# Optimization experiments

Measured on AMD Instinct MI355X. Metric: run time of the kernel, lower is better.

Reference implementation:

```python
import jax, jax.numpy as jnp
import numpy as np

B, T, V, E, H, NT = 64, 512, 8000, 256, 512, 4
HD = H // 2  # hidden per direction


def setup_inputs() -> dict:
    key = jax.random.key(0)
    ks = jax.random.split(key, 14)
    s = 0.1
    length = jnp.sort(jax.random.randint(ks[0], (B,), T // 2, T + 1))[::-1]  # sorted desc (pack_padded)
    mask = (jnp.arange(T)[None, :] < length[:, None]).astype(jnp.int32)
    sentence = jax.random.randint(ks[1], (B, T), 1, V + 1) * mask  # pad positions -> padding_idx 0
    tags = jax.random.randint(ks[2], (B, T), 0, NT)
    embedding = (jax.random.normal(ks[3], (V + 1, E)) * s).at[0].set(0.0)  # padding_idx row = 0
    w_ih_f = jax.random.normal(ks[4], (4 * HD, E)) * s
    w_hh_f = jax.random.normal(ks[5], (4 * HD, HD)) * s
    b_f = jax.random.normal(ks[6], (4 * HD,)) * s  # b_ih + b_hh combined
    w_ih_b = jax.random.normal(ks[7], (4 * HD, E)) * s
    w_hh_b = jax.random.normal(ks[8], (4 * HD, HD)) * s
    b_b = jax.random.normal(ks[9], (4 * HD,)) * s
    w_out = jax.random.normal(ks[10], (NT, H)) * s
    b_out = jnp.zeros((NT,), jnp.float32)
    start_trans = jax.random.uniform(ks[11], (NT,), minval=-0.1, maxval=0.1)
    end_trans = jax.random.uniform(ks[12], (NT,), minval=-0.1, maxval=0.1)
    trans = jax.random.uniform(ks[13], (NT, NT), minval=-0.1, maxval=0.1)
    return {"sentence": sentence, "tags": tags, "mask": mask, "length": length,
            "embedding": embedding, "w_ih_f": w_ih_f, "w_hh_f": w_hh_f, "b_f": b_f,
            "w_ih_b": w_ih_b, "w_hh_b": w_hh_b, "b_b": b_b,
            "w_out": w_out, "b_out": b_out,
            "start_trans": start_trans, "end_trans": end_trans, "trans": trans}


def _lstm_dir(x, maskf, w_ih, w_hh, b, reverse):
    # x: [B,T,E]; masked LSTM == packed LSTM (zero init state, padded outputs = 0)
    xg = jnp.einsum('bte,ge->btg', x, w_ih) + b           # [B,T,4HD]
    xg = jnp.swapaxes(xg, 0, 1)                           # [T,B,4HD]
    mt = jnp.swapaxes(maskf, 0, 1)[..., None]             # [T,B,1]
    h0 = jnp.zeros((x.shape[0], w_hh.shape[1]), x.dtype)

    def step(carry, inp):
        h, c = carry
        g, m = inp
        gates = g + h @ w_hh.T
        i, f, gg, o = jnp.split(gates, 4, axis=-1)  # torch gate order: i, f, g, o
        i = jax.nn.sigmoid(i); f = jax.nn.sigmoid(f)
        gg = jnp.tanh(gg); o = jax.nn.sigmoid(o)
        cn = f * c + i * gg
        hn = o * jnp.tanh(cn)
        h = m * hn + (1.0 - m) * h
        c = m * cn + (1.0 - m) * c
        return (h, c), h * m

    _, hs = jax.lax.scan(step, (h0, h0), (xg, mt), reverse=reverse)
    return jnp.swapaxes(hs, 0, 1)  # [B,T,HD]


def reference(sentence, tags, mask, length, embedding, w_ih_f, w_hh_f, b_f,
              w_ih_b, w_hh_b, b_b, w_out, b_out, start_trans, end_trans, trans):
    maskf = mask.astype(embedding.dtype)
    embeds = embedding[sentence]                           # [B,T,E] (dropout: eval/identity)
    hf = _lstm_dir(embeds, maskf, w_ih_f, w_hh_f, b_f, False)
    hb = _lstm_dir(embeds, maskf, w_ih_b, w_hh_b, b_b, True)
    feats = jnp.concatenate([hf, hb], -1) @ w_out.T + b_out  # [B,T,NT]

    # --- CRF log-likelihood (torchcrf), reduction='mean'; loss = -mean llh ---
    bsz = tags.shape[0]
    emit = jnp.take_along_axis(feats, tags[..., None], -1)[..., 0]   # [B,T]
    trans_sc = trans[tags[:, :-1], tags[:, 1:]]                       # [B,T-1]
    num = start_trans[tags[:, 0]] + emit[:, 0] \
        + jnp.sum(maskf[:, 1:] * (emit[:, 1:] + trans_sc), axis=1)
    last_tag = tags[jnp.arange(bsz), length - 1]
    num = num + end_trans[last_tag]

    ft = jnp.swapaxes(feats, 0, 1)                  # [T,B,NT]
    mt = jnp.swapaxes(maskf, 0, 1)[..., None]       # [T,B,1]
    alpha0 = start_trans[None, :] + ft[0]

    def step(alpha, inp):
        e, m = inp
        new = jax.nn.logsumexp(alpha[:, :, None] + trans[None] + e[:, None, :], axis=1)
        return m * new + (1.0 - m) * alpha, None

    alpha, _ = jax.lax.scan(step, alpha0, (ft[1:], mt[1:]))
    logZ = jax.nn.logsumexp(alpha + end_trans[None, :], axis=1)
    return -jnp.mean(num - logZ)
```

## Files before the change

kernel.cpp:

```cpp
#include <hip/hip_runtime.h>
#include <stdint.h>

#define BB 64
#define TT 512
#define EE 256
#define GG 1024
#define HDIM 256
#define NTAG 4

typedef _Float16 f16;
typedef _Float16 half8 __attribute__((ext_vector_type(8)));
typedef float floatx4 __attribute__((ext_vector_type(4)));

__device__ __forceinline__ int dot4i8(int a, int b, int c) {
#if __has_builtin(__builtin_amdgcn_sdot4)
  return __builtin_amdgcn_sdot4(a, b, c, false);
#else
  c += (int)(signed char)(a & 0xff)         * (int)(signed char)(b & 0xff);
  c += (int)(signed char)((a >> 8) & 0xff)  * (int)(signed char)((b >> 8) & 0xff);
  c += (int)(signed char)((a >> 16) & 0xff) * (int)(signed char)((b >> 16) & 0xff);
  c += (int)(signed char)((a >> 24) & 0xff) * (int)(signed char)((b >> 24) & 0xff);
  return c;
#endif
}

__device__ __forceinline__ float sigm(float x) {
  x = fminf(fmaxf(x, -30.f), 30.f);
  return 1.f / (1.f + __expf(-x));
}
__device__ __forceinline__ float tanh_f(float x) {
  x = fminf(fmaxf(x, -15.f), 15.f);
  float e = __expf(-2.f * x);
  return (1.f - e) / (1.f + e);
}

__global__ void pack_kernel(const float* __restrict__ wihf, const float* __restrict__ wihb,
                            const float* __restrict__ whhf, const float* __restrict__ whhb,
                            f16* __restrict__ bmat, uint32_t* __restrict__ whhp,
                            float* __restrict__ swhh) {
  int wv = (blockIdx.x * 256 + threadIdx.x) >> 6;
  int lane = threadIdx.x & 63;
  if (wv >= 2048) return;
  int dir = wv >> 10;
  int g = wv & 1023;
  const float* wih = dir ? wihb : wihf;
  const float* src = wih + (size_t)g * EE + lane * 4;
  f16* bp = bmat + (size_t)wv * EE + lane * 4;
  floatx4 v = *(const floatx4*)src;
  bp[0] = (f16)v[0]; bp[1] = (f16)v[1]; bp[2] = (f16)v[2]; bp[3] = (f16)v[3];
  const float* whh = dir ? whhb : whhf;
  floatx4 w = *(const floatx4*)(whh + (size_t)g * EE + lane * 4);
  float am = fmaxf(fmaxf(fabsf(w[0]), fabsf(w[1])), fmaxf(fabsf(w[2]), fabsf(w[3])));
#pragma unroll
  for (int d = 1; d < 64; d <<= 1) am = fmaxf(am, __shfl_xor(am, d));
  float s = am * (1.f / 127.f);
  float inv = am > 0.f ? 127.f / am : 0.f;
  int q0 = (int)rintf(w[0] * inv);
  int q1 = (int)rintf(w[1] * inv);
  int q2 = (int)rintf(w[2] * inv);
  int q3 = (int)rintf(w[3] * inv);
  uint32_t p = (uint32_t)(q0 & 255) | ((uint32_t)(q1 & 255) << 8) |
               ((uint32_t)(q2 & 255) << 16) | ((uint32_t)(q3 & 255) << 24);
  whhp[dir * 65536 + lane * 1024 + g] = p;
  if (lane == 0) swhh[dir * 1024 + g] = s;
}

__global__ __launch_bounds__(256) void gemm_kernel(
    const int* __restrict__ sentence, const float* __restrict__ embedding,
    const f16* __restrict__ bmat, f16* __restrict__ xgF, f16* __restrict__ xgB,
    int t0f, int t0b, int L, int Lsh) {
  __shared__ __attribute__((aligned(16))) f16 As[128][72];
  __shared__ __attribute__((aligned(16))) f16 Bs[128][72];
  int rt = blockIdx.x;
  int nt = blockIdx.y;
  int tid = threadIdx.x;
  int lane = tid & 63;
  int wv = tid >> 6;
  int BL = BB * L;
  int rbase = rt * 128;
  int half = (rbase >= BL) ? 1 : 0;
  int rloc0 = rbase - half * BL;
  int t0 = half ? t0b : t0f;

  floatx4 acc[4][4];
#pragma unroll
  for (int i = 0; i < 4; ++i)
#pragma unroll
    for (int j = 0; j < 4; ++j) acc[i][j] = (floatx4){0.f, 0.f, 0.f, 0.f};

  int ar = tid >> 1;
  int part = tid & 1;
  int rl = rloc0 + ar;
  int b_ = rl >> Lsh;
  int dt = rl & (L - 1);
  int t_ = t0 + dt;
  int sidx = sentence[b_ * TT + t_];
  const float* arow = embedding + (size_t)sidx * EE + part * 32;
  const f16* brow = bmat + ((size_t)(half * 1024 + nt * 128 + ar)) * EE + part * 32;
  int wm = (wv >> 1) * 64, wn = (wv & 1) * 64;

  for (int kk = 0; kk < 4; ++kk) {
    int k0 = kk * 64;
#pragma unroll
    for (int i = 0; i < 4; ++i) {
      floatx4 a0 = *(const floatx4*)(arow + k0 + i * 8);
      floatx4 a1 = *(const floatx4*)(arow + k0 + i * 8 + 4);
      union { f16 h[8]; uint4 u; } cv;
      cv.h[0] = (f16)a0[0]; cv.h[1] = (f16)a0[1]; cv.h[2] = (f16)a0[2]; cv.h[3] = (f16)a0[3];
      cv.h[4] = (f16)a1[0]; cv.h[5] = (f16)a1[1]; cv.h[6] = (f16)a1[2]; cv.h[7] = (f16)a1[3];
      *(uint4*)(&As[ar][part * 32 + i * 8]) = cv.u;
    }
#pragma unroll
    for (int i = 0; i < 4; ++i) {
      uint4 bv = *(const uint4*)(brow + k0 + i * 8);
      *(uint4*)(&Bs[ar][part * 32 + i * 8]) = bv;
    }
    __syncthreads();
#pragma unroll
    for (int kf = 0; kf < 2; ++kf) {
      int ko = kf * 32 + (lane >> 4) * 8;
      half8 af[4], bf[4];
#pragma unroll
      for (int mi = 0; mi < 4; ++mi)
        af[mi] = *(const half8*)(&As[wm + mi * 16 + (lane & 15)][ko]);
#pragma unroll
      for (int ni = 0; ni < 4; ++ni)
        bf[ni] = *(const half8*)(&Bs[wn + ni * 16 + (lane & 15)][ko]);
#pragma unroll
      for (int mi = 0; mi < 4; ++mi)
#pragma unroll
        for (int ni = 0; ni < 4; ++ni)
          acc[mi][ni] = __builtin_amdgcn_mfma_f32_16x16x32_f16(af[mi], bf[ni], acc[mi][ni], 0, 0, 0);
    }
    __syncthreads();
  }
  f16* out = half ? xgB : xgF;
#pragma unroll
  for (int mi = 0; mi < 4; ++mi) {
#pragma unroll
    for (int ni = 0; ni < 4; ++ni) {
      int rowl = wm + mi * 16 + (lane >> 4) * 4;
      int coll = nt * 128 + wn + ni * 16 + (lane & 15);
#pragma unroll
      for (int r = 0; r < 4; ++r) {
        out[(size_t)(rloc0 + rowl + r) * 1024 + coll] = (f16)acc[mi][ni][r];
      }
    }
  }
}

__global__ __launch_bounds__(512, 2) void rec_kernel(
    const int* __restrict__ length, const f16* __restrict__ xgF, const f16* __restrict__ xgB,
    const uint32_t* __restrict__ whhp, const float* __restrict__ swhh,
    const float* __restrict__ b_f, const float* __restrict__ b_b,
    const float* __restrict__ w_out, float* __restrict__ featf, float* __restrict__ featb,
    float* __restrict__ hstate, float* __restrict__ cstate,
    int t0f, int t0b, int L, int first) {
  __shared__ __attribute__((aligned(16))) uint32_t hq4[64];
  __shared__ float gacts[1024];
  __shared__ float fpart[4][4];

  int wid = blockIdx.x;
  int b = wid >> 1, dir = wid & 1;
  int tid = threadIdx.x;
  int lane = tid & 63;
  int wv = tid >> 6;
  int g0 = tid, g1 = tid + 512;
  int len = length[b];

  uint32_t wr0[64], wr1[64];
  const uint32_t* wp = whhp + dir * 65536;
#pragma unroll
  for (int q = 0; q < 64; ++q) { wr0[q] = wp[q * 1024 + g0]; wr1[q] = wp[q * 1024 + g1]; }
  float sw0 = swhh[dir * 1024 + g0] * (1.f / 127.f);
  float sw1 = swhh[dir * 1024 + g1] * (1.f / 127.f);
  const float* bias = dir ? b_b : b_f;
  float bi0 = bias[g0], bi1 = bias[g1];

  float wo0 = 0.f, wo1 = 0.f, wo2 = 0.f, wo3 = 0.f;
  float h = 0.f, c = 0.f;
  if (tid < 256) {
    wo0 = w_out[0 * 512 + dir * 256 + tid];
    wo1 = w_out[1 * 512 + dir * 256 + tid];
    wo2 = w_out[2 * 512 + dir * 256 + tid];
    wo3 = w_out[3 * 512 + dir * 256 + tid];
    if (!first) {
      h = hstate[(dir * BB + b) * HDIM + tid];
      c = cstate[(dir * BB + b) * HDIM + tid];
    }
  }
  float* featX = dir ? featb : featf;
  const f16* xg = dir ? xgB : xgF;

  if (tid < 256) {
    int q = (int)rintf(h * 127.f);
    q = max(-127, min(127, q));
    int qb1 = __shfl(q, (lane + 1) & 63);
    int qb2 = __shfl(q, (lane + 2) & 63);
    int qb3 = __shfl(q, (lane + 3) & 63);
    if ((lane & 3) == 0)
      hq4[tid >> 2] = (uint32_t)(q & 255) | ((uint32_t)(qb1 & 255) << 8) |
                      ((uint32_t)(qb2 & 255) << 16) | ((uint32_t)(qb3 & 255) << 24);
  }

  int tlo = dir ? t0b : t0f;
  int thi = min(tlo + L, len);
  int zstart = thi > tlo ? thi : tlo;
  int zcount = (tlo + L - zstart) * 4;
  size_t zbase = ((size_t)b * TT + zstart) * 4;
  for (int u = tid; u < zcount; u += 512) featX[zbase + u] = 0.f;
  __syncthreads();

  auto step = [&](int t) {
    size_t xoff = ((size_t)(b * L + (t - tlo)) << 10);
    float xv0 = (float)xg[xoff + g0];
    float xv1 = (float)xg[xoff + g1];
    uint32_t hq[64];
#pragma unroll
    for (int q2 = 0; q2 < 16; ++q2) {
      uint4 v = *((const uint4*)hq4 + q2);
      hq[q2 * 4 + 0] = v.x; hq[q2 * 4 + 1] = v.y; hq[q2 * 4 + 2] = v.z; hq[q2 * 4 + 3] = v.w;
    }
    int a0 = 0, a1 = 0;
#pragma unroll
    for (int q = 0; q < 64; ++q) {
      a0 = dot4i8(wr0[q], hq[q], a0);
      a1 = dot4i8(wr1[q], hq[q], a1);
    }
    float p0 = xv0 + bi0 + sw0 * (float)a0;
    float p1 = xv1 + bi1 + sw1 * (float)a1;
    float act0 = sigm(p0);
    float act1 = (tid < 256) ? tanh_f(p1) : sigm(p1);
    gacts[g0] = act0;
    gacts[g1] = act1;
    __syncthreads();
    if (tid < 256) {
      float iv = gacts[tid], fv = gacts[tid + 256], gv = gacts[tid + 512], ov = gacts[tid + 768];
      c = fv * c + iv * gv;
      h = ov * tanh_f(c);
      int q = (int)rintf(h * 127.f);
      q = max(-127, min(127, q));
      int qb1 = __shfl(q, (lane + 1) & 63);
      int qb2 = __shfl(q, (lane + 2) & 63);
      int qb3 = __shfl(q, (lane + 3) & 63);
      if ((lane & 3) == 0)
        hq4[tid >> 2] = (uint32_t)(q & 255) | ((uint32_t)(qb1 & 255) << 8) |
                        ((uint32_t)(qb2 & 255) << 16) | ((uint32_t)(qb3 & 255) << 24);
      float p0f = h * wo0, p1f = h * wo1, p2f = h * wo2, p3f = h * wo3;
#pragma unroll
      for (int d = 1; d < 64; d <<= 1) {
        p0f += __shfl_xor(p0f, d);
        p1f += __shfl_xor(p1f, d);
        p2f += __shfl_xor(p2f, d);
        p3f += __shfl_xor(p3f, d);
      }
      if (lane == 0) { fpart[wv][0] = p0f; fpart[wv][1] = p1f; fpart[wv][2] = p2f; fpart[wv][3] = p3f; }
    }
    __syncthreads();
    if (tid < 4) {
      featX[((size_t)b * TT + t) * 4 + tid] =
          fpart[0][tid] + fpart[1][tid] + fpart[2][tid] + fpart[3][tid];
    }
  };

  if (dir == 0) {
    for (int t = tlo; t < thi; ++t) step(t);
  } else {
    for (int t = thi - 1; t >= tlo; --t) step(t);
  }

  if (tid < 256) {
    hstate[(dir * BB + b) * HDIM + tid] = h;
    cstate[(dir * BB + b) * HDIM + tid] = c;
  }
}

__global__ void crf_kernel(const int* __restrict__ tags, const int* __restrict__ length,
                           const float* __restrict__ featf, const float* __restrict__ featb,
                           const float* __restrict__ b_out, const float* __restrict__ start_trans,
                           const float* __restrict__ end_trans, const float* __restrict__ trans,
                           float* __restrict__ res) {
  int b = blockIdx.x;
  int lane = threadIdx.x;
  int len = length[b];
  float bo = lane < NTAG ? b_out[lane] : 0.f;
  float tr0 = lane < NTAG ? trans[0 * 4 + lane] : 0.f;
  float tr1 = lane < NTAG ? trans[1 * 4 + lane] : 0.f;
  float tr2 = lane < NTAG ? trans[2 * 4 + lane] : 0.f;
  float tr3 = lane < NTAG ? trans[3 * 4 + lane] : 0.f;
  float st = lane < NTAG ? start_trans[lane] : 0.f;
  float en = lane < NTAG ? end_trans[lane] : 0.f;
  const int* tg = tags + b * TT;

  float e = 0.f;
  if (lane < NTAG)
    e = featf[((size_t)b * TT) * 4 + lane] + featb[((size_t)b * TT) * 4 + lane] + bo;
  int prev = tg[0];
  float alpha = st + e;
  float num = __shfl(st, prev) + __shfl(e, prev);
  for (int t = 1; t < len; ++t) {
    if (lane < NTAG)
      e = featf[((size_t)b * TT + t) * 4 + lane] + featb[((size_t)b * TT + t) * 4 + lane] + bo;
    float a0 = __shfl(alpha, 0), a1 = __shfl(alpha, 1), a2 = __shfl(alpha, 2), a3 = __shfl(alpha, 3);
    float v0 = a0 + tr0, v1 = a1 + tr1, v2 = a2 + tr2, v3 = a3 + tr3;
    float mx = fmaxf(fmaxf(v0, v1), fmaxf(v2, v3));
    float sm = __expf(v0 - mx) + __expf(v1 - mx) + __expf(v2 - mx) + __expf(v3 - mx);
    float anew = mx + __logf(sm) + e;
    int cur = tg[t];
    num += __shfl(e, cur) + trans[prev * 4 + cur];
    alpha = anew;
    prev = cur;
  }
  num += __shfl(en, prev);
  float v = alpha + en;
  float z0 = __shfl(v, 0), z1 = __shfl(v, 1), z2 = __shfl(v, 2), z3 = __shfl(v, 3);
  float mx = fmaxf(fmaxf(z0, z1), fmaxf(z2, z3));
  float logZ = mx + __logf(__expf(z0 - mx) + __expf(z1 - mx) + __expf(z2 - mx) + __expf(z3 - mx));
  if (lane == 0) res[b] = num - logZ;
}

__global__ void loss_kernel(const float* __restrict__ res, float* __restrict__ out) {
  int lane = threadIdx.x;
  float v = res[lane];
#pragma unroll
  for (int d = 1; d < 64; d <<= 1) v += __shfl_xor(v, d);
  if (lane == 0) out[0] = -v * (1.f / 64.f);
}

extern "C" void kernel_launch(void* const* d_in, const int* in_sizes, int n_in,
                              void* d_out, int out_size, void* d_ws, size_t ws_size,
                              hipStream_t stream) {
  (void)in_sizes; (void)n_in; (void)out_size;
  const int* sentence = (const int*)d_in[0];
  const int* tags = (const int*)d_in[1];
  const int* length = (const int*)d_in[3];
  const float* embedding = (const float*)d_in[4];
  const float* w_ih_f = (const float*)d_in[5];
  const float* w_hh_f = (const float*)d_in[6];
  const float* b_f = (const float*)d_in[7];
  const float* w_ih_b = (const float*)d_in[8];
  const float* w_hh_b = (const float*)d_in[9];
  const float* b_b = (const float*)d_in[10];
  const float* w_out = (const float*)d_in[11];
  const float* b_out = (const float*)d_in[12];
  const float* start_trans = (const float*)d_in[13];
  const float* end_trans = (const float*)d_in[14];
  const float* trans = (const float*)d_in[15];

  char* ws = (char*)d_ws;
  size_t off = 0;
  auto take = [&](size_t bytes) -> char* {
    char* p = ws + off;
    off = (off + bytes + 255) & ~(size_t)255;
    return p;
  };
  f16* bmat = (f16*)take((size_t)2048 * 256 * 2);
  uint32_t* whhp = (uint32_t*)take((size_t)2 * 64 * 1024 * 4);
  float* swhh = (float*)take((size_t)2 * 1024 * 4);
  float* featf = (float*)take((size_t)BB * TT * NTAG * 4);
  float* featb = (float*)take((size_t)BB * TT * NTAG * 4);
  float* hstate = (float*)take((size_t)2 * BB * HDIM * 4);
  float* cstate = (float*)take((size_t)2 * BB * HDIM * 4);
  float* res = (float*)take(256);
  size_t fixed = off;

  int L = TT, Lsh = 9;
  while (L > 32 && fixed + (size_t)BB * L * 1024 * 4 > ws_size) { L >>= 1; Lsh--; }
  f16* xgF = (f16*)take((size_t)BB * L * 1024 * 2);
  f16* xgB = (f16*)take((size_t)BB * L * 1024 * 2);
  int NC = TT / L;

  hipLaunchKernelGGL(pack_kernel, dim3(512), dim3(256), 0, stream,
                     w_ih_f, w_ih_b, w_hh_f, w_hh_b, bmat, whhp, swhh);

  for (int cidx = 0; cidx < NC; ++cidx) {
    int t0f_ = cidx * L;
    int t0b_ = TT - (cidx + 1) * L;
    hipLaunchKernelGGL(gemm_kernel, dim3(2 * BB * L / 128, 8), dim3(256), 0, stream,
                       sentence, embedding, bmat, xgF, xgB, t0f_, t0b_, L, Lsh);
    hipLaunchKernelGGL(rec_kernel, dim3(128), dim3(512), 0, stream,
                       length, xgF, xgB, whhp, swhh, b_f, b_b, w_out,
                       featf, featb, hstate, cstate, t0f_, t0b_, L, cidx == 0 ? 1 : 0);
  }
  hipLaunchKernelGGL(crf_kernel, dim3(BB), dim3(64), 0, stream,
                     tags, length, featf, featb, b_out, start_trans, end_trans, trans, res);
  hipLaunchKernelGGL(loss_kernel, dim3(1), dim3(64), 0, stream, res, (float*)d_out);
}
```

Measured before the change: 1.012 ms.

## Restructure LSTM recurrence to one thread per hidden unit, split output projection

```diff
diff --git a/kernel.cpp b/kernel.cpp
--- a/kernel.cpp
+++ b/kernel.cpp
@@ -4,23 +4,20 @@
 #define BB 64
 #define TT 512
 #define EE 256
-#define GG 1024
-#define HDIM 256
 #define NTAG 4
 
 typedef _Float16 f16;
 typedef _Float16 half8 __attribute__((ext_vector_type(8)));
+typedef _Float16 f16x4 __attribute__((ext_vector_type(4)));
 typedef float floatx4 __attribute__((ext_vector_type(4)));
 
-__device__ __forceinline__ int dot4i8(int a, int b, int c) {
+__device__ __forceinline__ int dot4i8(uint32_t a, uint32_t b, int c) {
 #if __has_builtin(__builtin_amdgcn_sdot4)
-  return __builtin_amdgcn_sdot4(a, b, c, false);
+  return __builtin_amdgcn_sdot4((int)a, (int)b, c, false);
 #else
-  c += (int)(signed char)(a & 0xff)         * (int)(signed char)(b & 0xff);
-  c += (int)(signed char)((a >> 8) & 0xff)  * (int)(signed char)((b >> 8) & 0xff);
-  c += (int)(signed char)((a >> 16) & 0xff) * (int)(signed char)((b >> 16) & 0xff);
-  c += (int)(signed char)((a >> 24) & 0xff) * (int)(signed char)((b >> 24) & 0xff);
-  return c;
+  int r;
+  asm("v_dot4_i32_i8 %0, %1, %2, %3" : "=v"(r) : "v"(a), "v"(b), "v"(c));
+  return r;
 #endif
 }
 
@@ -42,12 +39,14 @@
   int lane = threadIdx.x & 63;
   if (wv >= 2048) return;
   int dir = wv >> 10;
-  int g = wv & 1023;
+  int outr = wv & 1023;
+  int srcg = (outr & 3) * 256 + (outr >> 2);
   const float* wih = dir ? wihb : wihf;
-  const float* src = wih + (size_t)g * EE + lane * 4;
+  const float* src = wih + (size_t)srcg * EE + lane * 4;
   f16* bp = bmat + (size_t)wv * EE + lane * 4;
   floatx4 v = *(const floatx4*)src;
   bp[0] = (f16)v[0]; bp[1] = (f16)v[1]; bp[2] = (f16)v[2]; bp[3] = (f16)v[3];
+  int g = outr;
   const float* whh = dir ? whhb : whhf;
   floatx4 w = *(const floatx4*)(whh + (size_t)g * EE + lane * 4);
   float am = fmaxf(fmaxf(fabsf(w[0]), fabsf(w[1])), fmaxf(fabsf(w[2]), fabsf(w[3])));
@@ -149,166 +148,155 @@
   }
 }
 
-__global__ __launch_bounds__(512, 2) void rec_kernel(
+__global__ __launch_bounds__(256, 1) void rec_kernel(
     const int* __restrict__ length, const f16* __restrict__ xgF, const f16* __restrict__ xgB,
     const uint32_t* __restrict__ whhp, const float* __restrict__ swhh,
     const float* __restrict__ b_f, const float* __restrict__ b_b,
-    const float* __restrict__ w_out, float* __restrict__ featf, float* __restrict__ featb,
+    f16* __restrict__ hsF, f16* __restrict__ hsB,
     float* __restrict__ hstate, float* __restrict__ cstate,
     int t0f, int t0b, int L, int first) {
-  __shared__ __attribute__((aligned(16))) uint32_t hq4[64];
-  __shared__ float gacts[1024];
-  __shared__ float fpart[4][4];
-
+  __shared__ __attribute__((aligned(16))) uint32_t hq4[2][64];
   int wid = blockIdx.x;
   int b = wid >> 1, dir = wid & 1;
-  int tid = threadIdx.x;
-  int lane = tid & 63;
-  int wv = tid >> 6;
-  int g0 = tid, g1 = tid + 512;
+  int j = threadIdx.x;
   int len = length[b];
 
-  uint32_t wr0[64], wr1[64];
   const uint32_t* wp = whhp + dir * 65536;
-#pragma unroll
-  for (int q = 0; q < 64; ++q) { wr0[q] = wp[q * 1024 + g0]; wr1[q] = wp[q * 1024 + g1]; }
-  float sw0 = swhh[dir * 1024 + g0] * (1.f / 127.f);
-  float sw1 = swhh[dir * 1024 + g1] * (1.f / 127.f);
+  uint32_t wr0[64], wr1[64], wr2[64], wr3[64];
+#pragma unroll
+  for (int q = 0; q < 64; ++q) {
+    wr0[q] = wp[q * 1024 + j];
+    wr1[q] = wp[q * 1024 + 256 + j];
+    wr2[q] = wp[q * 1024 + 512 + j];
+    wr3[q] = wp[q * 1024 + 768 + j];
+  }
+  const float* sb = swhh + dir * 1024;
+  float sw0 = sb[j] * (1.f / 127.f), sw1 = sb[256 + j] * (1.f / 127.f);
+  float sw2 = sb[512 + j] * (1.f / 127.f), sw3 = sb[768 + j] * (1.f / 127.f);
   const float* bias = dir ? b_b : b_f;
-  float bi0 = bias[g0], bi1 = bias[g1];
-
-  float wo0 = 0.f, wo1 = 0.f, wo2 = 0.f, wo3 = 0.f;
+  float bi0 = bias[j], bi1 = bias[256 + j], bi2 = bias[512 + j], bi3 = bias[768 + j];
+
   float h = 0.f, c = 0.f;
-  if (tid < 256) {
-    wo0 = w_out[0 * 512 + dir * 256 + tid];
-    wo1 = w_out[1 * 512 + dir * 256 + tid];
-    wo2 = w_out[2 * 512 + dir * 256 + tid];
-    wo3 = w_out[3 * 512 + dir * 256 + tid];
-    if (!first) {
-      h = hstate[(dir * BB + b) * HDIM + tid];
-      c = cstate[(dir * BB + b) * HDIM + tid];
-    }
-  }
-  float* featX = dir ? featb : featf;
+  if (!first) {
+    h = hstate[(dir * BB + b) * 256 + j];
+    c = cstate[(dir * BB + b) * 256 + j];
+  }
   const f16* xg = dir ? xgB : xgF;
-
-  if (tid < 256) {
+  f16* hs = dir ? hsB : hsF;
+
+  int qi = (int)rintf(h * 127.f);
+  qi = max(-127, min(127, qi));
+  ((uint8_t*)&hq4[0][0])[j] = (uint8_t)qi;
+  __syncthreads();
+
+  int tlo = dir ? t0b : t0f;
+  int thi = min(tlo + L, len);
+  int nsteps = thi - tlo;
+  int p = 0;
+  for (int ii = 0; ii < nsteps; ++ii) {
+    int t = dir ? (thi - 1 - ii) : (tlo + ii);
+    f16x4 xv = *(const f16x4*)(xg + (((size_t)(b * L + (t - tlo))) << 10) + j * 4);
+    int A00 = 0, A01 = 0, A10 = 0, A11 = 0, A20 = 0, A21 = 0, A30 = 0, A31 = 0;
+#pragma unroll
+    for (int k = 0; k < 16; ++k) {
+      uint4 v = *((const uint4*)&hq4[p][0] + k);
+      A00 = dot4i8(wr0[4 * k + 0], v.x, A00); A01 = dot4i8(wr0[4 * k + 1], v.y, A01);
+      A00 = dot4i8(wr0[4 * k + 2], v.z, A00); A01 = dot4i8(wr0[4 * k + 3], v.w, A01);
+      A10 = dot4i8(wr1[4 * k + 0], v.x, A10); A11 = dot4i8(wr1[4 * k + 1], v.y, A11);
+      A10 = dot4i8(wr1[4 * k + 2], v.z, A10); A11 = dot4i8(wr1[4 * k + 3], v.w, A11);
+      A20 = dot4i8(wr2[4 * k + 0], v.x, A20); A21 = dot4i8(wr2[4 * k + 1], v.y, A21);
+      A20 = dot4i8(wr2[4 * k + 2], v.z, A20); A21 = dot4i8(wr2[4 * k + 3], v.w, A21);
+      A30 = dot4i8(wr3[4 * k + 0], v.x, A30); A31 = dot4i8(wr3[4 * k + 1], v.y, A31);
+      A30 = dot4i8(wr3[4 * k + 2], v.z, A30); A31 = dot4i8(wr3[4 * k + 3], v.w, A31);
+    }
+    float pi = (float)xv[0] + bi0 + sw0 * (float)(A00 + A01);
+    float pf = (float)xv[1] + bi1 + sw1 * (float)(A10 + A11);
+    float pg = (float)xv[2] + bi2 + sw2 * (float)(A20 + A21);
+    float po = (float)xv[3] + bi3 + sw3 * (float)(A30 + A31);
+    float iv = sigm(pi), fv = sigm(pf), gv = tanh_f(pg), ov = sigm(po);
+    c = fv * c + iv * gv;
+    h = ov * tanh_f(c);
+    hs[(((size_t)(b * TT + t)) << 8) + j] = (f16)h;
     int q = (int)rintf(h * 127.f);
     q = max(-127, min(127, q));
-    int qb1 = __shfl(q, (lane + 1) & 63);
-    int qb2 = __shfl(q, (lane + 2) & 63);
-    int qb3 = __shfl(q, (lane + 3) & 63);
-    if ((lane & 3) == 0)
-      hq4[tid >> 2] = (uint32_t)(q & 255) | ((uint32_t)(qb1 & 255) << 8) |
-                      ((uint32_t)(qb2 & 255) << 16) | ((uint32_t)(qb3 & 255) << 24);
-  }
-
-  int tlo = dir ? t0b : t0f;
-  int thi = min(tlo + L, len);
-  int zstart = thi > tlo ? thi : tlo;
-  int zcount = (tlo + L - zstart) * 4;
-  size_t zbase = ((size_t)b * TT + zstart) * 4;
-  for (int u = tid; u < zcount; u += 512) featX[zbase + u] = 0.f;
-  __syncthreads();
-
-  auto step = [&](int t) {
-    size_t xoff = ((size_t)(b * L + (t - tlo)) << 10);
-    float xv0 = (float)xg[xoff + g0];
-    float xv1 = (float)xg[xoff + g1];
-    uint32_t hq[64];
-#pragma unroll
-    for (int q2 = 0; q2 < 16; ++q2) {
-      uint4 v = *((const uint4*)hq4 + q2);
-      hq[q2 * 4 + 0] = v.x; hq[q2 * 4 + 1] = v.y; hq[q2 * 4 + 2] = v.z; hq[q2 * 4 + 3] = v.w;
-    }
-    int a0 = 0, a1 = 0;
-#pragma unroll
-    for (int q = 0; q < 64; ++q) {
-      a0 = dot4i8(wr0[q], hq[q], a0);
-      a1 = dot4i8(wr1[q], hq[q], a1);
-    }
-    float p0 = xv0 + bi0 + sw0 * (float)a0;
-    float p1 = xv1 + bi1 + sw1 * (float)a1;
-    float act0 = sigm(p0);
-    float act1 = (tid < 256) ? tanh_f(p1) : sigm(p1);
-    gacts[g0] = act0;
-    gacts[g1] = act1;
+    ((uint8_t*)&hq4[p ^ 1][0])[j] = (uint8_t)q;
     __syncthreads();
-    if (tid < 256) {
-      float iv = gacts[tid], fv = gacts[tid + 256], gv = gacts[tid + 512], ov = gacts[tid + 768];
-      c = fv * c + iv * gv;
-      h = ov * tanh_f(c);
-      int q = (int)rintf(h * 127.f);
-      q = max(-127, min(127, q));
-      int qb1 = __shfl(q, (lane + 1) & 63);
-      int qb2 = __shfl(q, (lane + 2) & 63);
-      int qb3 = __shfl(q, (lane + 3) & 63);
-      if ((lane & 3) == 0)
-        hq4[tid >> 2] = (uint32_t)(q & 255) | ((uint32_t)(qb1 & 255) << 8) |
-                        ((uint32_t)(qb2 & 255) << 16) | ((uint32_t)(qb3 & 255) << 24);
-      float p0f = h * wo0, p1f = h * wo1, p2f = h * wo2, p3f = h * wo3;
-#pragma unroll
-      for (int d = 1; d < 64; d <<= 1) {
-        p0f += __shfl_xor(p0f, d);
-        p1f += __shfl_xor(p1f, d);
-        p2f += __shfl_xor(p2f, d);
-        p3f += __shfl_xor(p3f, d);
-      }
-      if (lane == 0) { fpart[wv][0] = p0f; fpart[wv][1] = p1f; fpart[wv][2] = p2f; fpart[wv][3] = p3f; }
-    }
-    __syncthreads();
-    if (tid < 4) {
-      featX[((size_t)b * TT + t) * 4 + tid] =
-          fpart[0][tid] + fpart[1][tid] + fpart[2][tid] + fpart[3][tid];
-    }
-  };
-
-  if (dir == 0) {
-    for (int t = tlo; t < thi; ++t) step(t);
-  } else {
-    for (int t = thi - 1; t >= tlo; --t) step(t);
-  }
-
-  if (tid < 256) {
-    hstate[(dir * BB + b) * HDIM + tid] = h;
-    cstate[(dir * BB + b) * HDIM + tid] = c;
+    p ^= 1;
+  }
+  hstate[(dir * BB + b) * 256 + j] = h;
+  cstate[(dir * BB + b) * 256 + j] = c;
+}
+
+__global__ __launch_bounds__(256) void feats_kernel(
+    const f16* __restrict__ hsF, const f16* __restrict__ hsB,
+    const float* __restrict__ w_out, const float* __restrict__ b_out,
+    float* __restrict__ feats) {
+  int gw = (blockIdx.x * 256 + threadIdx.x) >> 6;
+  int lane = threadIdx.x & 63;
+  int nw = (gridDim.x * 256) >> 6;
+  float w0[8], w1[8], w2[8], w3[8];
+#pragma unroll
+  for (int u = 0; u < 8; ++u) {
+    w0[u] = w_out[0 * 512 + lane * 8 + u];
+    w1[u] = w_out[1 * 512 + lane * 8 + u];
+    w2[u] = w_out[2 * 512 + lane * 8 + u];
+    w3[u] = w_out[3 * 512 + lane * 8 + u];
+  }
+  float bo0 = b_out[0], bo1 = b_out[1], bo2 = b_out[2], bo3 = b_out[3];
+  const f16* src0 = (lane < 32) ? (hsF + lane * 8) : (hsB + (lane - 32) * 8);
+  for (int row = gw; row < BB * TT; row += nw) {
+    union { uint4 u; f16 h[8]; } hv;
+    hv.u = *(const uint4*)(src0 + ((size_t)row << 8));
+    float a0 = 0.f, a1 = 0.f, a2 = 0.f, a3 = 0.f;
+#pragma unroll
+    for (int u2 = 0; u2 < 8; ++u2) {
+      float x = (float)hv.h[u2];
+      a0 += x * w0[u2]; a1 += x * w1[u2]; a2 += x * w2[u2]; a3 += x * w3[u2];
+    }
+#pragma unroll
+    for (int d = 1; d < 64; d <<= 1) {
+      a0 += __shfl_xor(a0, d); a1 += __shfl_xor(a1, d);
+      a2 += __shfl_xor(a2, d); a3 += __shfl_xor(a3, d);
+    }
+    if (lane == 0) {
+      floatx4 o = {a0 + bo0, a1 + bo1, a2 + bo2, a3 + bo3};
+      *(floatx4*)(feats + (size_t)row * 4) = o;
+    }
   }
 }
 
 __global__ void crf_kernel(const int* __restrict__ tags, const int* __restrict__ length,
-                           const float* __restrict__ featf, const float* __restrict__ featb,
-                           const float* __restrict__ b_out, const float* __restrict__ start_trans,
+                           const float* __restrict__ feats,
+                           const float* __restrict__ start_trans,
                            const float* __restrict__ end_trans, const float* __restrict__ trans,
                            float* __restrict__ res) {
   int b = blockIdx.x;
   int lane = threadIdx.x;
   int len = length[b];
-  float bo = lane < NTAG ? b_out[lane] : 0.f;
-  float tr0 = lane < NTAG ? trans[0 * 4 + lane] : 0.f;
-  float tr1 = lane < NTAG ? trans[1 * 4 + lane] : 0.f;
-  float tr2 = lane < NTAG ? trans[2 * 4 + lane] : 0.f;
-  float tr3 = lane < NTAG ? trans[3 * 4 + lane] : 0.f;
-  float st = lane < NTAG ? start_trans[lane] : 0.f;
-  float en = lane < NTAG ? end_trans[lane] : 0.f;
+  float tr0 = lane < 4 ? trans[0 * 4 + lane] : 0.f;
+  float tr1 = lane < 4 ? trans[1 * 4 + lane] : 0.f;
+  float tr2 = lane < 4 ? trans[2 * 4 + lane] : 0.f;
+  float tr3 = lane < 4 ? trans[3 * 4 + lane] : 0.f;
+  float treg = lane < 16 ? trans[lane] : 0.f;
+  float st = lane < 4 ? start_trans[lane] : 0.f;
+  float en = lane < 4 ? end_trans[lane] : 0.f;
   const int* tg = tags + b * TT;
-
-  float e = 0.f;
-  if (lane < NTAG)
-    e = featf[((size_t)b * TT) * 4 + lane] + featb[((size_t)b * TT) * 4 + lane] + bo;
+  const float* fb = feats + (size_t)b * TT * 4;
+
+  float e = lane < 4 ? fb[lane] : 0.f;
   int prev = tg[0];
   float alpha = st + e;
-  float num = __shfl(st, prev) + __shfl(e, prev);
+  float num = __shfl(st + e, prev);
+#pragma unroll 2
   for (int t = 1; t < len; ++t) {
-    if (lane < NTAG)
-      e = featf[((size_t)b * TT + t) * 4 + lane] + featb[((size_t)b * TT + t) * 4 + lane] + bo;
+    float et = lane < 4 ? fb[t * 4 + lane] : 0.f;
+    int cur = tg[t];
     float a0 = __shfl(alpha, 0), a1 = __shfl(alpha, 1), a2 = __shfl(alpha, 2), a3 = __shfl(alpha, 3);
     float v0 = a0 + tr0, v1 = a1 + tr1, v2 = a2 + tr2, v3 = a3 + tr3;
     float mx = fmaxf(fmaxf(v0, v1), fmaxf(v2, v3));
     float sm = __expf(v0 - mx) + __expf(v1 - mx) + __expf(v2 - mx) + __expf(v3 - mx);
-    float anew = mx + __logf(sm) + e;
-    int cur = tg[t];
-    num += __shfl(e, cur) + trans[prev * 4 + cur];
-    alpha = anew;
+    alpha = mx + __logf(sm) + et;
+    num += __shfl(et, cur) + __shfl(treg, prev * 4 + cur);
     prev = cur;
   }
   num += __shfl(en, prev);
@@ -357,15 +345,16 @@
   f16* bmat = (f16*)take((size_t)2048 * 256 * 2);
   uint32_t* whhp = (uint32_t*)take((size_t)2 * 64 * 1024 * 4);
   float* swhh = (float*)take((size_t)2 * 1024 * 4);
-  float* featf = (float*)take((size_t)BB * TT * NTAG * 4);
-  float* featb = (float*)take((size_t)BB * TT * NTAG * 4);
-  float* hstate = (float*)take((size_t)2 * BB * HDIM * 4);
-  float* cstate = (float*)take((size_t)2 * BB * HDIM * 4);
+  f16* hsF = (f16*)take((size_t)BB * TT * 256 * 2);
+  f16* hsB = (f16*)take((size_t)BB * TT * 256 * 2);
+  float* feats = (float*)take((size_t)BB * TT * NTAG * 4);
+  float* hstate = (float*)take((size_t)2 * BB * 256 * 4);
+  float* cstate = (float*)take((size_t)2 * BB * 256 * 4);
   float* res = (float*)take(256);
   size_t fixed = off;
 
   int L = TT, Lsh = 9;
-  while (L > 32 && fixed + (size_t)BB * L * 1024 * 4 > ws_size) { L >>= 1; Lsh--; }
+  while (L > 32 && fixed + (size_t)BB * L * 1024 * 2 * 2 > ws_size) { L >>= 1; Lsh--; }
   f16* xgF = (f16*)take((size_t)BB * L * 1024 * 2);
   f16* xgB = (f16*)take((size_t)BB * L * 1024 * 2);
   int NC = TT / L;
@@ -378,11 +367,13 @@
     int t0b_ = TT - (cidx + 1) * L;
     hipLaunchKernelGGL(gemm_kernel, dim3(2 * BB * L / 128, 8), dim3(256), 0, stream,
                        sentence, embedding, bmat, xgF, xgB, t0f_, t0b_, L, Lsh);
-    hipLaunchKernelGGL(rec_kernel, dim3(128), dim3(512), 0, stream,
-                       length, xgF, xgB, whhp, swhh, b_f, b_b, w_out,
-                       featf, featb, hstate, cstate, t0f_, t0b_, L, cidx == 0 ? 1 : 0);
-  }
+    hipLaunchKernelGGL(rec_kernel, dim3(128), dim3(256), 0, stream,
+                       length, xgF, xgB, whhp, swhh, b_f, b_b, hsF, hsB,
+                       hstate, cstate, t0f_, t0b_, L, cidx == 0 ? 1 : 0);
+  }
+  hipLaunchKernelGGL(feats_kernel, dim3(512), dim3(256), 0, stream,
+                     hsF, hsB, w_out, b_out, feats);
   hipLaunchKernelGGL(crf_kernel, dim3(BB), dim3(64), 0, stream,
-                     tags, length, featf, featb, b_out, start_trans, end_trans, trans, res);
+                     tags, length, feats, start_trans, end_trans, trans, res);
   hipLaunchKernelGGL(loss_kernel, dim3(1), dim3(64), 0, stream, res, (float*)d_out);
 }
```

New measurement: 1.126 ms. +11.3%, slower.
